# Optimization experiments

Measured on AMD Instinct MI355X. Metric: run time of the kernel, lower is better.

The kernel has to match this reference:

```python
import jax, jax.numpy as jnp
import numpy as np

N = 1024      # n_nodes
F = 64        # n_features
L = 64        # lookback_window (must equal F for U1 @ B to typecheck, as in the torch code)
NDF = 4       # n_data_features
NTF = 8       # n_time_features
FC1 = 1024
FC2 = 512
K = 2         # kernel_size
DIL = (2, 2)  # dilation_list
DELTA = 0.05
EPS = 1e-5


def _ln(x, g, b):
    mu = x.mean(-1, keepdims=True)
    v = ((x - mu) ** 2).mean(-1, keepdims=True)
    return (x - mu) / jnp.sqrt(v + EPS) * g + b


def _mlp2(x, W1, b1, g, bb, W2, b2):
    h = jax.nn.relu(_ln(x @ W1 + b1, g, bb))
    return h @ W2 + b2


def setup_inputs() -> dict:
    ks = jax.random.split(jax.random.key(0), 16)
    def rn(i, shape, s=1.0):
        return jax.random.normal(ks[i], shape, dtype=jnp.float32) * s
    z = lambda *s: jnp.zeros(s, jnp.float32)
    o = lambda *s: jnp.ones(s, jnp.float32)
    return {
        "observation": rn(0, (N, NDF, L)),
        "time_features": rn(1, (L, NTF)),
        "layer_initial": rn(2, (L, N)),
        "sW1": rn(3, (N, 256), N ** -0.5), "sb1": z(256), "s_ln_g": o(256), "s_ln_b": z(256),
        "sW2": rn(4, (256, N * F), 256 ** -0.5), "sb2": z(N * F),
        "tW1": rn(5, (NTF, 256), NTF ** -0.5), "tb1": z(256), "t_ln_g": o(256), "t_ln_b": z(256),
        "tW2": rn(6, (256, N * F), 256 ** -0.5), "tb2": z(N * F),
        "B": o(F, F),
        "fW1": rn(7, (N * NDF, FC1), (N * NDF) ** -0.5), "fb1": z(FC1), "f1g": o(FC1), "f1b": z(FC1),
        "fW2": rn(8, (FC1, FC2), FC1 ** -0.5), "fb2": z(FC2), "f2g": o(FC2), "f2b": z(FC2),
        "fW3": rn(9, (FC2, N * F), FC2 ** -0.5), "fb3": z(N * F),
        "Wf": rn(10, (K, F, F)), "Wb": rn(11, (K, F, F)), "bconv": rn(12, (F,)),
    }


def _forward(observation, time_features, layer_initial, sW1, sb1, s_ln_g, s_ln_b, sW2, sb2,
             tW1, tb1, t_ln_g, t_ln_b, tW2, tb2, B,
             fW1, fb1, f1g, f1b, fW2, fb2, f2g, f2b, fW3, fb3, Wf, Wb, bconv):
    # GraphConstructor node embedding; U[:, :, j] is (N, L)
    emb = _mlp2(layer_initial, sW1, sb1, s_ln_g, s_ln_b, sW2, sb2) \
        + _mlp2(time_features, tW1, tb1, t_ln_g, t_ln_b, tW2, tb2)   # (L, N*F)
    U = emb.reshape(L, N, F).transpose(1, 0, 2)                      # (N, L, F)
    Uf = jnp.moveaxis(U, 2, 0)                                       # (F, N, L) for feature-axis gathers

    def adj(aidx, bidx):
        # batched adjacency: softmax over rows of thresholded U1 B U2^T, then D^-1/2 A D^-1/2
        Ua, Ub = Uf[aidx], Uf[bidx]                                  # (M, N, L)
        S = jax.lax.stop_gradient(jnp.einsum('mnl,lp,mqp->mnq', Ua, B, Ub))  # .detach() in torch
        S = jnp.where(S >= DELTA, S, 0.0)
        A = jax.nn.softmax(S, axis=-1)
        dn = 1.0 / jnp.sqrt(A.sum(-1))                               # degree is diagonal -> sqrtm/inverse = elementwise
        return A * dn[:, :, None] * dn[:, None, :]

    # fully_connected: observation (N, NDF, L) -> X (N, F, L)
    obs = observation.transpose(2, 0, 1).reshape(L, N * NDF)
    h = jax.nn.relu(_ln(obs @ fW1 + fb1, f1g, f1b))
    h = jax.nn.relu(_ln(h @ fW2 + fb2, f2g, f2b))
    X = (h @ fW3 + fb3).reshape(L, N, F).transpose(1, 2, 0)          # (N, F, L)

    gamma = 1
    outs = []
    for d in DIL:
        length = X.shape[-1]
        ts = np.arange(d - 1, length, d)                             # t with (t+1) % d == 0, static
        Z = jnp.zeros((ts.size, N, F), X.dtype)
        for k in range(K):
            tk = ts - k                                              # >= 0 since K <= min(DIL)
            Xk = X[:, :, tk]                                         # (N, F, M)
            A1 = adj((gamma * tk) % L, (gamma * ts) % L)             # pair (idx - k*gamma, idx)
            A2 = adj((gamma * ts) % L, (gamma * tk) % L)             # pair (idx, idx - k*gamma)
            msg = jnp.einsum('mnq,qfm->mnf', A1, Xk) @ Wf[k] \
                + jnp.einsum('mnq,qfm->mnf', A2, Xk) @ Wb[k] + bconv
            Z = Z + jnp.tanh(msg)
        X = jnp.moveaxis(Z, 0, 2)                                    # (N, F, M) becomes next layer input
        outs.append(X[:, :, -1])
        gamma *= d
    return jnp.stack(outs)                                           # (len(DIL), N, F)


def reference(observation, time_features, layer_initial, sW1, sb1, s_ln_g, s_ln_b, sW2, sb2,
              tW1, tb1, t_ln_g, t_ln_b, tW2, tb2, B,
              fW1, fb1, f1g, f1b, fW2, fb2, f2g, f2b, fW3, fb3, Wf, Wb, bconv):
    return _forward(observation, time_features, layer_initial, sW1, sb1, s_ln_g, s_ln_b, sW2, sb2,
                    tW1, tb1, t_ln_g, t_ln_b, tW2, tb2, B,
                    fW1, fb1, f1g, f1b, fW2, fb2, f2g, f2b, fW3, fb3, Wf, Wb, bconv)
```

## Files before the change

kernel.cpp:

```cpp
#include <hip/hip_runtime.h>
#include <cstddef>

#define EPS_C   1e-5f
#define DELTA_C 0.05f

struct Pairs { int a[6]; int b[6]; int t[6]; };


template<int K>
__device__ __forceinline__ void head_body(
    const float* __restrict__ A, const float* __restrict__ W1,
    const float* __restrict__ b1, const float* __restrict__ g,
    const float* __restrict__ bb, float* __restrict__ H,
    float* As, float* rs, float* rs2, int row, int j)
{
  for (int i = j; i < K; i += 256) As[i] = A[row * K + i];
  __syncthreads();

  float a0 = 0.f;
  const float* __restrict__ Wp = W1 + j;
#pragma unroll
  for (int c = 0; c < K; ++c) a0 += As[c] * Wp[(size_t)c * 256];
  float acc = a0 + b1[j];

  rs[j] = acc; rs2[j] = acc * acc;
  __syncthreads();
  for (int st = 128; st > 0; st >>= 1) {
    if (j < st) { rs[j] += rs[j + st]; rs2[j] += rs2[j + st]; }
    __syncthreads();
  }
  float mu  = rs[0] * (1.f / 256.f);
  float var = rs2[0] * (1.f / 256.f) - mu * mu;
  float y = (acc - mu) * rsqrtf(var + EPS_C) * g[j] + bb[j];
  H[row * 256 + j] = fmaxf(y, 0.f);
}

template<int MODE>
__device__ __forceinline__ void skinny_body(
    const float* __restrict__ A, const float* __restrict__ W,
    float* __restrict__ part, int K, int N, int bid, int tid,
    float (*ARs)[64])
{
  int jblocks = N >> 8;
  int jb = bid % jblocks;
  int kc = bid / jblocks;
  int k0 = kc << 6;
  {
    int c = tid >> 6, i = tid & 63;
    int k = k0 + i;
    float v;
    if (MODE == 0) v = A[c * K + k];
    else { int n = k >> 2, df = k & 3; v = A[n * 256 + df * 64 + 60 + c]; }
    ARs[c][i] = v;
  }
  __syncthreads();
  int j = (jb << 8) + tid;
  float acc0 = 0.f, acc1 = 0.f, acc2 = 0.f, acc3 = 0.f;
#pragma unroll
  for (int kk = 0; kk < 64; kk += 16) {
    float w[16];
#pragma unroll
    for (int u = 0; u < 16; ++u) w[u] = W[(size_t)(k0 + kk + u) * N + j];
#pragma unroll
    for (int u = 0; u < 16; ++u) {
      acc0 += ARs[0][kk + u] * w[u];
      acc1 += ARs[1][kk + u] * w[u];
      acc2 += ARs[2][kk + u] * w[u];
      acc3 += ARs[3][kk + u] * w[u];
    }
  }
  part[(size_t)(kc * 4 + 0) * N + j] = acc0;
  part[(size_t)(kc * 4 + 1) * N + j] = acc1;
  part[(size_t)(kc * 4 + 2) * N + j] = acc2;
  part[(size_t)(kc * 4 + 3) * N + j] = acc3;
}

template<int N_, int PARTS>
__device__ __forceinline__ void red_body(
    const float* __restrict__ part, const float* __restrict__ bias,
    const float* __restrict__ g, const float* __restrict__ bb,
    float* __restrict__ out, int c, int tid, float* rs, float* rs2)
{
  constexpr int PER = N_ >> 8;
  float x[PER];
  float s = 0.f, s2 = 0.f;
#pragma unroll
  for (int i = 0; i < PER; ++i) {
    int j = (i << 8) + tid;
    float v = bias[j];
#pragma unroll 8
    for (int p = 0; p < PARTS; ++p) v += part[(size_t)(p * 4 + c) * N_ + j];
    x[i] = v; s += v; s2 += v * v;
  }
  rs[tid] = s; rs2[tid] = s2;
  __syncthreads();
  for (int st = 128; st > 0; st >>= 1) {
    if (tid < st) { rs[tid] += rs[tid + st]; rs2[tid] += rs2[tid + st]; }
    __syncthreads();
  }
  float mu  = rs[0] / (float)N_;
  float var = rs2[0] / (float)N_ - mu * mu;
  float inv = rsqrtf(var + EPS_C);
#pragma unroll
  for (int i = 0; i < PER; ++i) {
    int j = (i << 8) + tid;
    out[c * N_ + j] = fmaxf((x[i] - mu) * inv * g[j] + bb[j], 0.f);
  }
}


__global__ __launch_bounds__(256) void k1_heads_skinny(
    const float* __restrict__ layer_initial, const float* __restrict__ sW1,
    float* __restrict__ Hp,
    const float* __restrict__ time_features, const float* __restrict__ tW1,
    const float* __restrict__ tb1, const float* __restrict__ t_g,
    const float* __restrict__ t_b, float* __restrict__ Ht,
    const float* __restrict__ observation, const float* __restrict__ fW1,
    float* __restrict__ part1)
{
  __shared__ float As[256];
  __shared__ float rs[256], rs2[256];
  __shared__ float ARs[4][64];
  int bid = blockIdx.x, j = threadIdx.x;
  if (bid < 256) {
    int kc = bid >> 6, row = bid & 63;
    int k0 = kc << 8;
    As[j] = layer_initial[row * 1024 + k0 + j];
    __syncthreads();
    float a0 = 0.f, a1 = 0.f, a2 = 0.f, a3 = 0.f;
    const float* __restrict__ Wp = sW1 + (size_t)k0 * 256 + j;
#pragma unroll 2
    for (int c = 0; c < 256; c += 8) {
      float w0 = Wp[(size_t)(c + 0) * 256];
      float w1 = Wp[(size_t)(c + 1) * 256];
      float w2 = Wp[(size_t)(c + 2) * 256];
      float w3 = Wp[(size_t)(c + 3) * 256];
      float w4 = Wp[(size_t)(c + 4) * 256];
      float w5 = Wp[(size_t)(c + 5) * 256];
      float w6 = Wp[(size_t)(c + 6) * 256];
      float w7 = Wp[(size_t)(c + 7) * 256];
      a0 += As[c + 0] * w0 + As[c + 4] * w4;
      a1 += As[c + 1] * w1 + As[c + 5] * w5;
      a2 += As[c + 2] * w2 + As[c + 6] * w6;
      a3 += As[c + 3] * w3 + As[c + 7] * w7;
    }
    Hp[(size_t)(kc * 64 + row) * 256 + j] = (a0 + a1) + (a2 + a3);
  } else if (bid < 320) {
    head_body<8>(time_features, tW1, tb1, t_g, t_b, Ht, As, rs, rs2, bid - 256, j);
  } else {
    skinny_body<1>(observation, fW1, part1, 4096, 1024, bid - 320, j, ARs);
  }
}

__global__ __launch_bounds__(256) void k2_headred_red1(
    const float* __restrict__ Hp, const float* __restrict__ sb1,
    const float* __restrict__ s_g, const float* __restrict__ s_b,
    float* __restrict__ Hs,
    const float* __restrict__ part1, const float* __restrict__ fb1,
    const float* __restrict__ f1g, const float* __restrict__ f1b,
    float* __restrict__ h1)
{
  __shared__ float rs[256], rs2[256];
  int tid = threadIdx.x;
  if (blockIdx.x < 64) {
    int row = blockIdx.x;
    float acc = sb1[tid];
#pragma unroll
    for (int kc = 0; kc < 4; ++kc)
      acc += Hp[(size_t)(kc * 64 + row) * 256 + tid];
    rs[tid] = acc; rs2[tid] = acc * acc;
    __syncthreads();
    for (int st = 128; st > 0; st >>= 1) {
      if (tid < st) { rs[tid] += rs[tid + st]; rs2[tid] += rs2[tid + st]; }
      __syncthreads();
    }
    float mu  = rs[0] * (1.f / 256.f);
    float var = rs2[0] * (1.f / 256.f) - mu * mu;
    float y = (acc - mu) * rsqrtf(var + EPS_C) * s_g[tid] + s_b[tid];
    Hs[row * 256 + tid] = fmaxf(y, 0.f);
  } else {
    red_body<1024, 64>(part1, fb1, f1g, f1b, h1, blockIdx.x - 64, tid, rs, rs2);
  }
}

__global__ __launch_bounds__(256) void k3_emb_skinny(
    const float* __restrict__ Hs, const float* __restrict__ Ht,
    const float* __restrict__ sW2, const float* __restrict__ sb2,
    const float* __restrict__ tW2, const float* __restrict__ tb2,
    float* __restrict__ Vs,
    const float* __restrict__ h1, const float* __restrict__ fW2,
    float* __restrict__ part2)
{
  __shared__ __align__(16) float HcT[64][68];
  __shared__ __align__(16) float Wc[64][20];
  int tid = threadIdx.x;
  if (blockIdx.x < 256) {
    int n0 = blockIdx.x * 4;
    int lq = tid >> 4, jc = tid & 15;
    int nn = n0 + (jc >> 2), cc = jc & 3;
    int kkw = tid >> 2, nloc = tid & 3;

    float4 hr[4]; float4 wr;
    {
#pragma unroll
      for (int i = 0; i < 4; ++i) {
        int flat = i * 1024 + tid * 4;
        int l = flat >> 6, kk = flat & 63;
        hr[i] = *(const float4*)&Hs[l * 256 + kk];
      }
      wr = *(const float4*)&sW2[(size_t)kkw * 65536 + (size_t)(n0 + nloc) * 64 + 60];
    }
    float acc0 = 0.f, acc1 = 0.f, acc2 = 0.f, acc3 = 0.f;
    for (int ch = 0; ch < 8; ++ch) {
      __syncthreads();
#pragma unroll
      for (int i = 0; i < 4; ++i) {
        int flat = i * 1024 + tid * 4;
        int l = flat >> 6, kk = flat & 63;
        HcT[kk + 0][l] = hr[i].x;
        HcT[kk + 1][l] = hr[i].y;
        HcT[kk + 2][l] = hr[i].z;
        HcT[kk + 3][l] = hr[i].w;
      }
      *(float4*)&Wc[kkw][nloc * 4] = wr;
      __syncthreads();
      if (ch < 7) {
        int nc2 = ch + 1;
        const float* __restrict__ Hsrc = (nc2 < 4) ? Hs : Ht;
        const float* __restrict__ Wsrc = (nc2 < 4) ? sW2 : tW2;
        int kl = (nc2 & 3) << 6;
#pragma unroll
        for (int i = 0; i < 4; ++i) {
          int flat = i * 1024 + tid * 4;
          int l = flat >> 6, kk = flat & 63;
          hr[i] = *(const float4*)&Hsrc[l * 256 + kl + kk];
        }
        wr = *(const float4*)&Wsrc[(size_t)(kl + kkw) * 65536 + (size_t)(n0 + nloc) * 64 + 60];
      }
#pragma unroll 8
      for (int kk = 0; kk < 64; ++kk) {
        float4 av = *(const float4*)&HcT[kk][lq * 4];
        float w = Wc[kk][jc];
        acc0 += av.x * w; acc1 += av.y * w; acc2 += av.z * w; acc3 += av.w * w;
      }
    }
    int jj = nn * 64 + 60 + cc;
    float bias = sb2[jj] + tb2[jj];
    float4 st = { acc0 + bias, acc1 + bias, acc2 + bias, acc3 + bias };
    *(float4*)&Vs[(size_t)cc * 65536 + (size_t)nn * 64 + lq * 4] = st;
  } else {
    skinny_body<0>(h1, fW2, part2, 1024, 512, blockIdx.x - 256, tid,
                   (float(*)[64])&HcT[0][0]);
  }
}

__global__ __launch_bounds__(256) void k4_red2_vab(
    const float* __restrict__ part2, const float* __restrict__ fb2,
    const float* __restrict__ f2g, const float* __restrict__ f2b,
    float* __restrict__ h2,
    const float* __restrict__ Vs, const float* __restrict__ Bmat,
    float* __restrict__ VaBt, float* __restrict__ VsT)
{
  __shared__ float Va[64][65], Bs[64][65];
  int tid = threadIdx.x;
  if (blockIdx.x < 4) {
    red_body<512, 16>(part2, fb2, f2g, f2b, h2, blockIdx.x, tid,
                      &Va[0][0], &Bs[0][0]);
  } else {
    int bid = blockIdx.x - 4;
    int c = bid >> 4, nb = bid & 15;
    int n0 = nb << 6;
    int rg = tid >> 4, cg = tid & 15;
#pragma unroll
    for (int i = 0; i < 4; ++i) {
      int flat = i * 1024 + tid * 4;
      int rr = flat >> 6, cc = flat & 63;
      float4 v = *(const float4*)&Vs[(size_t)c * 65536 + (size_t)(n0 + rr) * 64 + cc];
      Va[rr][cc] = v.x; Va[rr][cc+1] = v.y; Va[rr][cc+2] = v.z; Va[rr][cc+3] = v.w;
      float4 w = *(const float4*)&Bmat[flat];
      Bs[rr][cc] = w.x; Bs[rr][cc+1] = w.y; Bs[rr][cc+2] = w.z; Bs[rr][cc+3] = w.w;
    }
    __syncthreads();
#pragma unroll
    for (int i = 0; i < 4; ++i) {
      int flat = i * 1024 + tid * 4;
      int l = flat >> 6, nn = flat & 63;
      float4 st = { Va[nn][l], Va[nn+1][l], Va[nn+2][l], Va[nn+3][l] };
      *(float4*)&VsT[(size_t)c * 65536 + (size_t)l * 1024 + n0 + nn] = st;
    }
    float acc[4][4];
#pragma unroll
    for (int i = 0; i < 4; ++i)
#pragma unroll
      for (int j = 0; j < 4; ++j) acc[i][j] = 0.f;
#pragma unroll 4
    for (int l = 0; l < 64; ++l) {
      float av[4], bv[4];
#pragma unroll
      for (int i = 0; i < 4; ++i) av[i] = Va[rg * 4 + i][l];
#pragma unroll
      for (int j = 0; j < 4; ++j) bv[j] = Bs[l][cg * 4 + j];
#pragma unroll
      for (int i = 0; i < 4; ++i)
#pragma unroll
        for (int j = 0; j < 4; ++j) acc[i][j] += av[i] * bv[j];
    }
#pragma unroll
    for (int j = 0; j < 4; ++j) {
      float4 st = { acc[0][j], acc[1][j], acc[2][j], acc[3][j] };
      *(float4*)&VaBt[(size_t)c * 65536 + (size_t)(cg * 4 + j) * 1024 + n0 + rg * 4] = st;
    }
  }
}

__global__ __launch_bounds__(256) void big_w3c(
    const float* __restrict__ h2, const float* __restrict__ fW3,
    const float* __restrict__ fb3, float* __restrict__ Xr)
{
  int tid = threadIdx.x;
  __shared__ float h2s[2048];
  __shared__ float sm[4][128];
  for (int i = tid; i < 2048; i += 256) h2s[i] = h2[i];
  int col = tid & 127, ks = tid >> 7;
  int j = blockIdx.x * 128 + col;
  int kbase = ks << 8;
  __syncthreads();
  float acc0 = 0.f, acc1 = 0.f, acc2 = 0.f, acc3 = 0.f;
  for (int k0 = 0; k0 < 256; k0 += 16) {
    float w[16];
#pragma unroll
    for (int u = 0; u < 16; ++u) w[u] = fW3[(size_t)(kbase + k0 + u) * 65536 + j];
#pragma unroll
    for (int u = 0; u < 16; ++u) {
      int k = kbase + k0 + u;
      acc0 += h2s[k]        * w[u];
      acc1 += h2s[512 + k]  * w[u];
      acc2 += h2s[1024 + k] * w[u];
      acc3 += h2s[1536 + k] * w[u];
    }
  }
  if (ks) { sm[0][col] = acc0; sm[1][col] = acc1; sm[2][col] = acc2; sm[3][col] = acc3; }
  __syncthreads();
  if (!ks) {
    float b = fb3[j];
    Xr[j]            = acc0 + sm[0][col] + b;
    Xr[65536 + j]    = acc1 + sm[1][col] + b;
    Xr[131072 + j]   = acc2 + sm[2][col] + b;
    Xr[196608 + j]   = acc3 + sm[3][col] + b;
  }
}

template<int NSPLIT>
__global__ __launch_bounds__(256) void attn_partial(
    const float* __restrict__ VaBt, const float* __restrict__ VsT,
    const float* __restrict__ Xbase, float* __restrict__ Pl,
    float* __restrict__ ml, Pairs pr)
{
  constexpr int TILES = 16 / NSPLIT;
  int pi  = blockIdx.x / (16 * NSPLIT);
  int rem = blockIdx.x % (16 * NSPLIT);
  int nb  = rem / NSPLIT;
  int s   = rem % NSPLIT;
  int n0  = nb << 6;
  int tid = threadIdx.x;
  int rg = tid >> 4, cg = tid & 15;
  int rg4 = rg * 4, cg4 = cg * 4;
  int a = pr.a[pi], b = pr.b[pi], t = pr.t[pi];

  __shared__ __align__(16) float VaT[64][68];
  __shared__ __align__(16) float VbT[64][68];
  __shared__ __align__(16) float Xs[64][68];
  float (*St)[68] = VbT;

#pragma unroll
  for (int i = 0; i < 4; ++i) {
    int flat = i * 1024 + tid * 4;
    int p = flat >> 6, nn = flat & 63;
    float4 v = *(const float4*)&VaBt[(size_t)a * 65536 + (size_t)p * 1024 + n0 + nn];
    *(float4*)&VaT[p][nn] = v;
  }
  float m_run[4], l_run[4];
#pragma unroll
  for (int i = 0; i < 4; ++i) { m_run[i] = -1e30f; l_run[i] = 0.f; }
  float P[4][4];
#pragma unroll
  for (int i = 0; i < 4; ++i)
#pragma unroll
    for (int j = 0; j < 4; ++j) P[i][j] = 0.f;
  __syncthreads();

  for (int ti = 0; ti < TILES; ++ti) {
    int q0 = (s * TILES + ti) << 6;
    if (ti) __syncthreads();
#pragma unroll
    for (int i = 0; i < 4; ++i) {
      int flat = i * 1024 + tid * 4;
      int p = flat >> 6, qq = flat & 63;
      float4 v = *(const float4*)&VsT[(size_t)b * 65536 + (size_t)p * 1024 + q0 + qq];
      *(float4*)&VbT[p][qq] = v;
      float4 x = *(const float4*)&Xbase[(size_t)t * 65536 + (size_t)(q0 + p) * 64 + qq];
      *(float4*)&Xs[p][qq] = x;
    }
    __syncthreads();
    float sa[4][4];
#pragma unroll
    for (int i = 0; i < 4; ++i)
#pragma unroll
      for (int j = 0; j < 4; ++j) sa[i][j] = 0.f;
#pragma unroll 4
    for (int p = 0; p < 64; ++p) {
      float av[4], bv[4];
      *(float4*)av = *(const float4*)&VaT[p][rg4];
      *(float4*)bv = *(const float4*)&VbT[p][cg4];
#pragma unroll
      for (int i = 0; i < 4; ++i)
#pragma unroll
        for (int j = 0; j < 4; ++j) sa[i][j] += av[i] * bv[j];
    }
    float scv[4];
#pragma unroll
    for (int i = 0; i < 4; ++i) {
#pragma unroll
      for (int j = 0; j < 4; ++j) sa[i][j] = (sa[i][j] >= DELTA_C) ? sa[i][j] : 0.f;
      float tm = fmaxf(fmaxf(sa[i][0], sa[i][1]), fmaxf(sa[i][2], sa[i][3]));
      tm = fmaxf(tm, __shfl_xor(tm, 1));
      tm = fmaxf(tm, __shfl_xor(tm, 2));
      tm = fmaxf(tm, __shfl_xor(tm, 4));
      tm = fmaxf(tm, __shfl_xor(tm, 8));
      float mnew = fmaxf(m_run[i], tm);
      float sc = __expf(m_run[i] - mnew);
      float ssum = 0.f;
#pragma unroll
      for (int j = 0; j < 4; ++j) {
        float e = __expf(sa[i][j] - mnew);
        sa[i][j] = e;
        ssum += e;
      }
      ssum += __shfl_xor(ssum, 1);
      ssum += __shfl_xor(ssum, 2);
      ssum += __shfl_xor(ssum, 4);
      ssum += __shfl_xor(ssum, 8);
      l_run[i] = l_run[i] * sc + ssum;
      m_run[i] = mnew;
      scv[i] = sc;
    }
    __syncthreads();
#pragma unroll
    for (int i = 0; i < 4; ++i) {
      float4 e4 = { sa[i][0], sa[i][1], sa[i][2], sa[i][3] };
      *(float4*)&St[rg4 + i][cg4] = e4;
    }
    __syncthreads();
#pragma unroll
    for (int i = 0; i < 4; ++i)
#pragma unroll
      for (int j = 0; j < 4; ++j) P[i][j] *= scv[i];
#pragma unroll 2
    for (int q4 = 0; q4 < 64; q4 += 4) {
      float4 ev[4], xv[4];
#pragma unroll
      for (int i = 0; i < 4; ++i) ev[i] = *(const float4*)&St[rg4 + i][q4];
#pragma unroll
      for (int u = 0; u < 4; ++u) xv[u] = *(const float4*)&Xs[q4 + u][cg4];
#pragma unroll
      for (int i = 0; i < 4; ++i) {
        const float* e = &ev[i].x;
#pragma unroll
        for (int u = 0; u < 4; ++u) {
          const float* x = &xv[u].x;
#pragma unroll
          for (int j = 0; j < 4; ++j) P[i][j] += e[u] * x[j];
        }
      }
    }
  }
  size_t base = (size_t)((pi * 16 + nb) * NSPLIT + s);
  float* pp = Pl + base * 4096;
#pragma unroll
  for (int i = 0; i < 4; ++i) {
    float4 st = { P[i][0], P[i][1], P[i][2], P[i][3] };
    *(float4*)&pp[(size_t)(rg4 + i) * 64 + cg4] = st;
  }
  if ((tid & 15) == 0) {
    float* mlp = ml + base * 128;
#pragma unroll
    for (int i = 0; i < 4; ++i) {
      mlp[rg4 + i]      = m_run[i];
      mlp[64 + rg4 + i] = l_run[i];
    }
  }
}

template<int NS_T>
__global__ __launch_bounds__(256) void merge_partial16(
    const float* __restrict__ Pl, const float* __restrict__ ml,
    const float* __restrict__ Wf, const float* __restrict__ Wb,
    float* __restrict__ Gp)
{
  int mm  = blockIdx.x / 192;
  int rem = blockIdx.x % 192;
  int nb  = rem / 12;
  int r2  = rem % 12;
  int nq  = r2 / 3, inst = r2 % 3;
  int tid = threadIdx.x;
  int r = tid >> 4, fq = tid & 15;

  __shared__ __align__(16) float Ps[16][68];
  __shared__ __align__(16) float Wt[64][68];

  size_t base = (size_t)((mm * 3 + inst) * 16 + nb) * NS_T;
  const float* mlp = ml + base * 128;
  int rowi = nq * 16 + r;
  float mg = -1e30f;
#pragma unroll
  for (int s2 = 0; s2 < NS_T; ++s2) mg = fmaxf(mg, mlp[s2 * 128 + rowi]);
  float acc[4] = {0.f, 0.f, 0.f, 0.f};
  float lg = 0.f;
#pragma unroll
  for (int s2 = 0; s2 < NS_T; ++s2) {
    float f = __expf(mlp[s2 * 128 + rowi] - mg);
    lg += f * mlp[s2 * 128 + 64 + rowi];
    float4 v = *(const float4*)(Pl + (base + s2) * 4096 + rowi * 64 + fq * 4);
    acc[0] += f * v.x; acc[1] += f * v.y; acc[2] += f * v.z; acc[3] += f * v.w;
  }
  float inv = 1.f / lg;
  float4 pv = { acc[0] * inv, acc[1] * inv, acc[2] * inv, acc[3] * inv };
  *(float4*)&Ps[r][fq * 4] = pv;
  for (int i = tid; i < 4096; i += 256) {
    int rr = i >> 6, cc = i & 63;
    float w;
    if (inst == 0)      w = Wf[i] + Wb[i];
    else if (inst == 1) w = Wf[4096 + i];
    else                w = Wb[4096 + i];
    Wt[rr][cc] = w;
  }
  __syncthreads();
  float g0 = 0.f, g1 = 0.f, g2 = 0.f, g3 = 0.f;
#pragma unroll 8
  for (int f = 0; f < 64; ++f) {
    float p = Ps[r][f];
    float4 w4 = *(const float4*)&Wt[f][fq * 4];
    g0 += p * w4.x; g1 += p * w4.y; g2 += p * w4.z; g3 += p * w4.w;
  }
  float4 st = { g0, g1, g2, g3 };
  *(float4*)&Gp[(size_t)(mm * 3 + inst) * 65536 +
                (size_t)(nb * 64 + nq * 16 + r) * 64 + fq * 4] = st;
}

__global__ __launch_bounds__(256) void finalize_z(
    const float* __restrict__ Gp, const float* __restrict__ bconv,
    float* __restrict__ dst0, float* __restrict__ dst1, float* __restrict__ extra1)
{
  int mm = blockIdx.x >> 4;
  int nb = blockIdx.x & 15;
  int tid = threadIdx.x;
  size_t tileOff = (size_t)(nb << 6) * 64;
  const float* g0 = Gp + (size_t)(mm * 3 + 0) * 65536 + tileOff;
  const float* g1 = Gp + (size_t)(mm * 3 + 1) * 65536 + tileOff;
  const float* g2 = Gp + (size_t)(mm * 3 + 2) * 65536 + tileOff;
  float* dst = (mm == 0) ? dst0 : dst1;
  for (int i = tid * 4; i < 4096; i += 1024) {
    float4 a = *(const float4*)&g0[i];
    float4 b = *(const float4*)&g1[i];
    float4 c = *(const float4*)&g2[i];
    int col = i & 63;
    float4 z;
    z.x = tanhf(a.x + bconv[col+0]) + tanhf(b.x + c.x + bconv[col+0]);
    z.y = tanhf(a.y + bconv[col+1]) + tanhf(b.y + c.y + bconv[col+1]);
    z.z = tanhf(a.z + bconv[col+2]) + tanhf(b.z + c.z + bconv[col+2]);
    z.w = tanhf(a.w + bconv[col+3]) + tanhf(b.w + c.w + bconv[col+3]);
    *(float4*)&dst[tileOff + i] = z;
    if (mm == 1 && extra1) *(float4*)&extra1[tileOff + i] = z;
  }
}

extern "C" void kernel_launch(void* const* d_in, const int* in_sizes, int n_in,
                              void* d_out, int out_size, void* d_ws, size_t ws_size,
                              hipStream_t stream)
{
  const float* observation   = (const float*)d_in[0];
  const float* time_features = (const float*)d_in[1];
  const float* layer_initial = (const float*)d_in[2];
  const float* sW1   = (const float*)d_in[3];
  const float* sb1   = (const float*)d_in[4];
  const float* s_ln_g = (const float*)d_in[5];
  const float* s_ln_b = (const float*)d_in[6];
  const float* sW2   = (const float*)d_in[7];
  const float* sb2   = (const float*)d_in[8];
  const float* tW1   = (const float*)d_in[9];
  const float* tb1   = (const float*)d_in[10];
  const float* t_ln_g = (const float*)d_in[11];
  const float* t_ln_b = (const float*)d_in[12];
  const float* tW2   = (const float*)d_in[13];
  const float* tb2   = (const float*)d_in[14];
  const float* Bmat  = (const float*)d_in[15];
  const float* fW1   = (const float*)d_in[16];
  const float* fb1   = (const float*)d_in[17];
  const float* f1g   = (const float*)d_in[18];
  const float* f1b   = (const float*)d_in[19];
  const float* fW2   = (const float*)d_in[20];
  const float* fb2   = (const float*)d_in[21];
  const float* f2g   = (const float*)d_in[22];
  const float* f2b   = (const float*)d_in[23];
  const float* fW3   = (const float*)d_in[24];
  const float* fb3   = (const float*)d_in[25];
  const float* Wf    = (const float*)d_in[26];
  const float* Wb    = (const float*)d_in[27];
  const float* bconv = (const float*)d_in[28];
  float* out = (float*)d_out;

  float* ws    = (float*)d_ws;
  float* Hs    = ws;
  float* Ht    = Hs    + 16384;
  float* Hp    = Ht    + 16384;
  float* Vs    = Hp    + 65536;
  float* VsT   = Vs    + 262144;
  float* VaBt  = VsT   + 262144;
  float* part1 = VaBt  + 262144;
  float* part2 = part1 + 262144;
  float* h1    = part2 + 32768;
  float* h2    = h1    + 4096;
  float* Xr    = h2    + 2048;
  float* Pl    = Xr    + 262144;
  float* ml    = Pl    + 3145728;
  float* Pl2   = ml    + 98304;
  float* ml2   = Pl2   + 3145728;
  float* Z1    = ml2   + 98304;
  float* Gp    = Z1    + 131072;

  k1_heads_skinny<<<576, 256, 0, stream>>>(
      layer_initial, sW1, Hp,
      time_features, tW1, tb1, t_ln_g, t_ln_b, Ht,
      observation, fW1, part1);
  k2_headred_red1<<<68, 256, 0, stream>>>(
      Hp, sb1, s_ln_g, s_ln_b, Hs,
      part1, fb1, f1g, f1b, h1);
  k3_emb_skinny<<<288, 256, 0, stream>>>(
      Hs, Ht, sW2, sb2, tW2, tb2, Vs, h1, fW2, part2);
  k4_red2_vab<<<68, 256, 0, stream>>>(
      part2, fb2, f2g, f2b, h2, Vs, Bmat, VaBt, VsT);
  big_w3c<<<512, 256, 0, stream>>>(h2, fW3, fb3, Xr);

  Pairs pA;
  pA.a[0]=1; pA.b[0]=1; pA.t[0]=1;
  pA.a[1]=0; pA.b[1]=1; pA.t[1]=0;
  pA.a[2]=1; pA.b[2]=0; pA.t[2]=0;
  pA.a[3]=3; pA.b[3]=3; pA.t[3]=3;
  pA.a[4]=2; pA.b[4]=3; pA.t[4]=2;
  pA.a[5]=3; pA.b[5]=2; pA.t[5]=2;
  attn_partial<8><<<6 * 16 * 8, 256, 0, stream>>>(VaBt, VsT, Xr, Pl, ml, pA);
  merge_partial16<8><<<384, 256, 0, stream>>>(Pl, ml, Wf, Wb, Gp);
  finalize_z<<<32, 256, 0, stream>>>(Gp, bconv, Z1, Z1 + 65536, out);

  Pairs pB;
  pB.a[0]=2; pB.b[0]=2; pB.t[0]=1;
  pB.a[1]=0; pB.b[1]=2; pB.t[1]=0;
  pB.a[2]=2; pB.b[2]=0; pB.t[2]=0;
  pB.a[3]=pB.a[4]=pB.a[5]=0; pB.b[3]=pB.b[4]=pB.b[5]=0; pB.t[3]=pB.t[4]=pB.t[5]=0;
  attn_partial<16><<<3 * 16 * 16, 256, 0, stream>>>(VaBt, VsT, Z1, Pl2, ml2, pB);
  merge_partial16<16><<<192, 256, 0, stream>>>(Pl2, ml2, Wf, Wb, Gp);
  finalize_z<<<16, 256, 0, stream>>>(Gp, bconv, out + 65536, nullptr, nullptr);
}
```

Before: 151.2 us.

## Widen attention thread tile to 4x8 and fuse merge with finalize

The attention partial kernel now runs 128 threads per block, each computing a 4x8 output micro-tile, which raises register reuse and cuts shared-memory loads per FMA. The per-instance merge and the tanh finalize kernels are fused into one kernel that loops over the three instances and writes Z directly. This removes a launch per layer and the Gp intermediate round trip through global memory. In exchange there are fewer threads per block and fewer merge blocks, which may reduce latency hiding and parallelism.

```diff
diff --git a/kernel.cpp b/kernel.cpp
--- a/kernel.cpp
+++ b/kernel.cpp
@@ -351,7 +351,7 @@
 }
 
 template<int NSPLIT>
-__global__ __launch_bounds__(256) void attn_partial(
+__global__ __launch_bounds__(128) void attn_partial(
     const float* __restrict__ VaBt, const float* __restrict__ VsT,
     const float* __restrict__ Xbase, float* __restrict__ Pl,
     float* __restrict__ ml, Pairs pr)
@@ -363,8 +363,9 @@
   int s   = rem % NSPLIT;
   int n0  = nb << 6;
   int tid = threadIdx.x;
-  int rg = tid >> 4, cg = tid & 15;
-  int rg4 = rg * 4, cg4 = cg * 4;
+  int rg = tid >> 3;
+  int cg = tid & 7;
+  int rg4 = rg * 4, cg8 = cg * 8;
   int a = pr.a[pi], b = pr.b[pi], t = pr.t[pi];
 
   __shared__ __align__(16) float VaT[64][68];
@@ -373,8 +374,8 @@
   float (*St)[68] = VbT;
 
 #pragma unroll
-  for (int i = 0; i < 4; ++i) {
-    int flat = i * 1024 + tid * 4;
+  for (int i = 0; i < 8; ++i) {
+    int flat = i * 512 + tid * 4;
     int p = flat >> 6, nn = flat & 63;
     float4 v = *(const float4*)&VaBt[(size_t)a * 65536 + (size_t)p * 1024 + n0 + nn];
     *(float4*)&VaT[p][nn] = v;
@@ -382,19 +383,19 @@
   float m_run[4], l_run[4];
 #pragma unroll
   for (int i = 0; i < 4; ++i) { m_run[i] = -1e30f; l_run[i] = 0.f; }
-  float P[4][4];
+  float P[4][8];
 #pragma unroll
   for (int i = 0; i < 4; ++i)
 #pragma unroll
-    for (int j = 0; j < 4; ++j) P[i][j] = 0.f;
+    for (int j = 0; j < 8; ++j) P[i][j] = 0.f;
   __syncthreads();
 
   for (int ti = 0; ti < TILES; ++ti) {
     int q0 = (s * TILES + ti) << 6;
     if (ti) __syncthreads();
 #pragma unroll
-    for (int i = 0; i < 4; ++i) {
-      int flat = i * 1024 + tid * 4;
+    for (int i = 0; i < 8; ++i) {
+      int flat = i * 512 + tid * 4;
       int p = flat >> 6, qq = flat & 63;
       float4 v = *(const float4*)&VsT[(size_t)b * 65536 + (size_t)p * 1024 + q0 + qq];
       *(float4*)&VbT[p][qq] = v;
@@ -402,36 +403,42 @@
       *(float4*)&Xs[p][qq] = x;
     }
     __syncthreads();
-    float sa[4][4];
+    float sa[4][8];
 #pragma unroll
     for (int i = 0; i < 4; ++i)
 #pragma unroll
-      for (int j = 0; j < 4; ++j) sa[i][j] = 0.f;
+      for (int j = 0; j < 8; ++j) sa[i][j] = 0.f;
 #pragma unroll 4
     for (int p = 0; p < 64; ++p) {
-      float av[4], bv[4];
+      float av[4], bl[4], bh[4];
       *(float4*)av = *(const float4*)&VaT[p][rg4];
-      *(float4*)bv = *(const float4*)&VbT[p][cg4];
-#pragma unroll
-      for (int i = 0; i < 4; ++i)
-#pragma unroll
-        for (int j = 0; j < 4; ++j) sa[i][j] += av[i] * bv[j];
+      *(float4*)bl = *(const float4*)&VbT[p][cg8];
+      *(float4*)bh = *(const float4*)&VbT[p][cg8 + 4];
+#pragma unroll
+      for (int i = 0; i < 4; ++i) {
+#pragma unroll
+        for (int j = 0; j < 4; ++j) {
+          sa[i][j]     += av[i] * bl[j];
+          sa[i][j + 4] += av[i] * bh[j];
+        }
+      }
     }
     float scv[4];
 #pragma unroll
     for (int i = 0; i < 4; ++i) {
 #pragma unroll
-      for (int j = 0; j < 4; ++j) sa[i][j] = (sa[i][j] >= DELTA_C) ? sa[i][j] : 0.f;
-      float tm = fmaxf(fmaxf(sa[i][0], sa[i][1]), fmaxf(sa[i][2], sa[i][3]));
+      for (int j = 0; j < 8; ++j) sa[i][j] = (sa[i][j] >= DELTA_C) ? sa[i][j] : 0.f;
+      float tm = sa[i][0];
+#pragma unroll
+      for (int j = 1; j < 8; ++j) tm = fmaxf(tm, sa[i][j]);
       tm = fmaxf(tm, __shfl_xor(tm, 1));
       tm = fmaxf(tm, __shfl_xor(tm, 2));
       tm = fmaxf(tm, __shfl_xor(tm, 4));
-      tm = fmaxf(tm, __shfl_xor(tm, 8));
       float mnew = fmaxf(m_run[i], tm);
       float sc = __expf(m_run[i] - mnew);
       float ssum = 0.f;
 #pragma unroll
-      for (int j = 0; j < 4; ++j) {
+      for (int j = 0; j < 8; ++j) {
         float e = __expf(sa[i][j] - mnew);
         sa[i][j] = e;
         ssum += e;
@@ -439,7 +446,6 @@
       ssum += __shfl_xor(ssum, 1);
       ssum += __shfl_xor(ssum, 2);
       ssum += __shfl_xor(ssum, 4);
-      ssum += __shfl_xor(ssum, 8);
       l_run[i] = l_run[i] * sc + ssum;
       m_run[i] = mnew;
       scv[i] = sc;
@@ -447,29 +453,39 @@
     __syncthreads();
 #pragma unroll
     for (int i = 0; i < 4; ++i) {
-      float4 e4 = { sa[i][0], sa[i][1], sa[i][2], sa[i][3] };
-      *(float4*)&St[rg4 + i][cg4] = e4;
+      float4 e0 = { sa[i][0], sa[i][1], sa[i][2], sa[i][3] };
+      float4 e1 = { sa[i][4], sa[i][5], sa[i][6], sa[i][7] };
+      *(float4*)&St[rg4 + i][cg8]     = e0;
+      *(float4*)&St[rg4 + i][cg8 + 4] = e1;
     }
     __syncthreads();
 #pragma unroll
     for (int i = 0; i < 4; ++i)
 #pragma unroll
-      for (int j = 0; j < 4; ++j) P[i][j] *= scv[i];
+      for (int j = 0; j < 8; ++j) P[i][j] *= scv[i];
 #pragma unroll 2
     for (int q4 = 0; q4 < 64; q4 += 4) {
-      float4 ev[4], xv[4];
+      float4 ev[4];
 #pragma unroll
       for (int i = 0; i < 4; ++i) ev[i] = *(const float4*)&St[rg4 + i][q4];
-#pragma unroll
-      for (int u = 0; u < 4; ++u) xv[u] = *(const float4*)&Xs[q4 + u][cg4];
+      float4 xl[4], xh[4];
+#pragma unroll
+      for (int u = 0; u < 4; ++u) {
+        xl[u] = *(const float4*)&Xs[q4 + u][cg8];
+        xh[u] = *(const float4*)&Xs[q4 + u][cg8 + 4];
+      }
 #pragma unroll
       for (int i = 0; i < 4; ++i) {
         const float* e = &ev[i].x;
 #pragma unroll
         for (int u = 0; u < 4; ++u) {
-          const float* x = &xv[u].x;
-#pragma unroll
-          for (int j = 0; j < 4; ++j) P[i][j] += e[u] * x[j];
+          const float* pl = &xl[u].x;
+          const float* ph = &xh[u].x;
+#pragma unroll
+          for (int j = 0; j < 4; ++j) {
+            P[i][j]     += e[u] * pl[j];
+            P[i][j + 4] += e[u] * ph[j];
+          }
         }
       }
     }
@@ -478,10 +494,12 @@
   float* pp = Pl + base * 4096;
 #pragma unroll
   for (int i = 0; i < 4; ++i) {
-    float4 st = { P[i][0], P[i][1], P[i][2], P[i][3] };
-    *(float4*)&pp[(size_t)(rg4 + i) * 64 + cg4] = st;
-  }
-  if ((tid & 15) == 0) {
+    float4 s0 = { P[i][0], P[i][1], P[i][2], P[i][3] };
+    float4 s1 = { P[i][4], P[i][5], P[i][6], P[i][7] };
+    *(float4*)&pp[(size_t)(rg4 + i) * 64 + cg8]     = s0;
+    *(float4*)&pp[(size_t)(rg4 + i) * 64 + cg8 + 4] = s1;
+  }
+  if (cg == 0) {
     float* mlp = ml + base * 128;
 #pragma unroll
     for (int i = 0; i < 4; ++i) {
@@ -492,86 +510,75 @@
 }
 
 template<int NS_T>
-__global__ __launch_bounds__(256) void merge_partial16(
+__global__ __launch_bounds__(256) void merge_fin3(
     const float* __restrict__ Pl, const float* __restrict__ ml,
     const float* __restrict__ Wf, const float* __restrict__ Wb,
-    float* __restrict__ Gp)
-{
-  int mm  = blockIdx.x / 192;
-  int rem = blockIdx.x % 192;
-  int nb  = rem / 12;
-  int r2  = rem % 12;
-  int nq  = r2 / 3, inst = r2 % 3;
+    const float* __restrict__ bconv,
+    float* __restrict__ dst0, float* __restrict__ dst1, float* __restrict__ extra1)
+{
+  int mm  = blockIdx.x >> 6;
+  int rem = blockIdx.x & 63;
+  int nb  = rem >> 2;
+  int nq  = rem & 3;
   int tid = threadIdx.x;
   int r = tid >> 4, fq = tid & 15;
+  int rowi = nq * 16 + r;
 
   __shared__ __align__(16) float Ps[16][68];
   __shared__ __align__(16) float Wt[64][68];
 
-  size_t base = (size_t)((mm * 3 + inst) * 16 + nb) * NS_T;
-  const float* mlp = ml + base * 128;
-  int rowi = nq * 16 + r;
-  float mg = -1e30f;
-#pragma unroll
-  for (int s2 = 0; s2 < NS_T; ++s2) mg = fmaxf(mg, mlp[s2 * 128 + rowi]);
-  float acc[4] = {0.f, 0.f, 0.f, 0.f};
-  float lg = 0.f;
-#pragma unroll
-  for (int s2 = 0; s2 < NS_T; ++s2) {
-    float f = __expf(mlp[s2 * 128 + rowi] - mg);
-    lg += f * mlp[s2 * 128 + 64 + rowi];
-    float4 v = *(const float4*)(Pl + (base + s2) * 4096 + rowi * 64 + fq * 4);
-    acc[0] += f * v.x; acc[1] += f * v.y; acc[2] += f * v.z; acc[3] += f * v.w;
-  }
-  float inv = 1.f / lg;
-  float4 pv = { acc[0] * inv, acc[1] * inv, acc[2] * inv, acc[3] * inv };
-  *(float4*)&Ps[r][fq * 4] = pv;
-  for (int i = tid; i < 4096; i += 256) {
-    int rr = i >> 6, cc = i & 63;
-    float w;
-    if (inst == 0)      w = Wf[i] + Wb[i];
-    else if (inst == 1) w = Wf[4096 + i];
-    else                w = Wb[4096 + i];
-    Wt[rr][cc] = w;
-  }
-  __syncthreads();
-  float g0 = 0.f, g1 = 0.f, g2 = 0.f, g3 = 0.f;
+  float z0[4] = {0.f, 0.f, 0.f, 0.f};
+  float z1[4] = {0.f, 0.f, 0.f, 0.f};
+
+  for (int inst = 0; inst < 3; ++inst) {
+    size_t base = (size_t)((mm * 3 + inst) * 16 + nb) * NS_T;
+    const float* mlp = ml + base * 128;
+    float mg = -1e30f;
+#pragma unroll
+    for (int s2 = 0; s2 < NS_T; ++s2) mg = fmaxf(mg, mlp[s2 * 128 + rowi]);
+    float acc[4] = {0.f, 0.f, 0.f, 0.f};
+    float lg = 0.f;
+#pragma unroll
+    for (int s2 = 0; s2 < NS_T; ++s2) {
+      float f = __expf(mlp[s2 * 128 + rowi] - mg);
+      lg += f * mlp[s2 * 128 + 64 + rowi];
+      float4 v = *(const float4*)(Pl + (base + s2) * 4096 + rowi * 64 + fq * 4);
+      acc[0] += f * v.x; acc[1] += f * v.y; acc[2] += f * v.z; acc[3] += f * v.w;
+    }
+    float inv = 1.f / lg;
+    if (inst) __syncthreads();
+    float4 pv = { acc[0] * inv, acc[1] * inv, acc[2] * inv, acc[3] * inv };
+    *(float4*)&Ps[r][fq * 4] = pv;
+    for (int i = tid; i < 4096; i += 256) {
+      int rr = i >> 6, cc = i & 63;
+      float w;
+      if (inst == 0)      w = Wf[i] + Wb[i];
+      else if (inst == 1) w = Wf[4096 + i];
+      else                w = Wb[4096 + i];
+      Wt[rr][cc] = w;
+    }
+    __syncthreads();
+    float g0 = 0.f, g1 = 0.f, g2 = 0.f, g3 = 0.f;
 #pragma unroll 8
-  for (int f = 0; f < 64; ++f) {
-    float p = Ps[r][f];
-    float4 w4 = *(const float4*)&Wt[f][fq * 4];
-    g0 += p * w4.x; g1 += p * w4.y; g2 += p * w4.z; g3 += p * w4.w;
-  }
-  float4 st = { g0, g1, g2, g3 };
-  *(float4*)&Gp[(size_t)(mm * 3 + inst) * 65536 +
-                (size_t)(nb * 64 + nq * 16 + r) * 64 + fq * 4] = st;
-}
-
-__global__ __launch_bounds__(256) void finalize_z(
-    const float* __restrict__ Gp, const float* __restrict__ bconv,
-    float* __restrict__ dst0, float* __restrict__ dst1, float* __restrict__ extra1)
-{
-  int mm = blockIdx.x >> 4;
-  int nb = blockIdx.x & 15;
-  int tid = threadIdx.x;
-  size_t tileOff = (size_t)(nb << 6) * 64;
-  const float* g0 = Gp + (size_t)(mm * 3 + 0) * 65536 + tileOff;
-  const float* g1 = Gp + (size_t)(mm * 3 + 1) * 65536 + tileOff;
-  const float* g2 = Gp + (size_t)(mm * 3 + 2) * 65536 + tileOff;
+    for (int f = 0; f < 64; ++f) {
+      float p = Ps[r][f];
+      float4 w4 = *(const float4*)&Wt[f][fq * 4];
+      g0 += p * w4.x; g1 += p * w4.y; g2 += p * w4.z; g3 += p * w4.w;
+    }
+    if (inst == 0) { z0[0] = g0; z0[1] = g1; z0[2] = g2; z0[3] = g3; }
+    else           { z1[0] += g0; z1[1] += g1; z1[2] += g2; z1[3] += g3; }
+  }
+
+  int col = fq * 4;
+  float4 z;
+  z.x = tanhf(z0[0] + bconv[col+0]) + tanhf(z1[0] + bconv[col+0]);
+  z.y = tanhf(z0[1] + bconv[col+1]) + tanhf(z1[1] + bconv[col+1]);
+  z.z = tanhf(z0[2] + bconv[col+2]) + tanhf(z1[2] + bconv[col+2]);
+  z.w = tanhf(z0[3] + bconv[col+3]) + tanhf(z1[3] + bconv[col+3]);
   float* dst = (mm == 0) ? dst0 : dst1;
-  for (int i = tid * 4; i < 4096; i += 1024) {
-    float4 a = *(const float4*)&g0[i];
-    float4 b = *(const float4*)&g1[i];
-    float4 c = *(const float4*)&g2[i];
-    int col = i & 63;
-    float4 z;
-    z.x = tanhf(a.x + bconv[col+0]) + tanhf(b.x + c.x + bconv[col+0]);
-    z.y = tanhf(a.y + bconv[col+1]) + tanhf(b.y + c.y + bconv[col+1]);
-    z.z = tanhf(a.z + bconv[col+2]) + tanhf(b.z + c.z + bconv[col+2]);
-    z.w = tanhf(a.w + bconv[col+3]) + tanhf(b.w + c.w + bconv[col+3]);
-    *(float4*)&dst[tileOff + i] = z;
-    if (mm == 1 && extra1) *(float4*)&extra1[tileOff + i] = z;
-  }
+  size_t idx = (size_t)(nb * 64 + rowi) * 64 + col;
+  *(float4*)&dst[idx] = z;
+  if (mm == 1 && extra1) *(float4*)&extra1[idx] = z;
 }
 
 extern "C" void kernel_launch(void* const* d_in, const int* in_sizes, int n_in,
@@ -626,7 +633,6 @@
   float* Pl2   = ml    + 98304;
   float* ml2   = Pl2   + 3145728;
   float* Z1    = ml2   + 98304;
-  float* Gp    = Z1    + 131072;
 
   k1_heads_skinny<<<576, 256, 0, stream>>>(
       layer_initial, sW1, Hp,
@@ -648,16 +654,16 @@
   pA.a[3]=3; pA.b[3]=3; pA.t[3]=3;
   pA.a[4]=2; pA.b[4]=3; pA.t[4]=2;
   pA.a[5]=3; pA.b[5]=2; pA.t[5]=2;
-  attn_partial<8><<<6 * 16 * 8, 256, 0, stream>>>(VaBt, VsT, Xr, Pl, ml, pA);
-  merge_partial16<8><<<384, 256, 0, stream>>>(Pl, ml, Wf, Wb, Gp);
-  finalize_z<<<32, 256, 0, stream>>>(Gp, bconv, Z1, Z1 + 65536, out);
+  attn_partial<8><<<6 * 16 * 8, 128, 0, stream>>>(VaBt, VsT, Xr, Pl, ml, pA);
+  merge_fin3<8><<<128, 256, 0, stream>>>(Pl, ml, Wf, Wb, bconv,
+                                         Z1, Z1 + 65536, out);
 
   Pairs pB;
   pB.a[0]=2; pB.b[0]=2; pB.t[0]=1;
   pB.a[1]=0; pB.b[1]=2; pB.t[1]=0;
   pB.a[2]=2; pB.b[2]=0; pB.t[2]=0;
   pB.a[3]=pB.a[4]=pB.a[5]=0; pB.b[3]=pB.b[4]=pB.b[5]=0; pB.t[3]=pB.t[4]=pB.t[5]=0;
-  attn_partial<16><<<3 * 16 * 16, 256, 0, stream>>>(VaBt, VsT, Z1, Pl2, ml2, pB);
-  merge_partial16<16><<<192, 256, 0, stream>>>(Pl2, ml2, Wf, Wb, Gp);
-  finalize_z<<<16, 256, 0, stream>>>(Gp, bconv, out + 65536, nullptr, nullptr);
-}
+  attn_partial<16><<<3 * 16 * 16, 128, 0, stream>>>(VaBt, VsT, Z1, Pl2, ml2, pB);
+  merge_fin3<16><<<64, 256, 0, stream>>>(Pl2, ml2, Wf, Wb, bconv,
+                                         out + 65536, nullptr, nullptr);
+}
```

New measurement: 163.9 us. 1.08x slower.
